# Performance work log

Measured on AMD Instinct MI355X. Metric: run time of the kernel, lower is better.

## Reference

```python
import jax, jax.numpy as jnp
import numpy as np

N = 50000   # nodes
E = 800000  # edges (avg degree 16)
DIMS = [(128, 128), (128, 128), (128, 64)]  # (in, out) per SAGEConv layer
EPS_BN = 1e-5
EPS_NORM = 1e-12


def _make_layer(key, din, dout):
    k1, k2 = jax.random.split(key)
    s = 1.0 / np.sqrt(din)
    return (
        jax.random.normal(k1, (dout, din), jnp.float32) * s,  # Wl: neighbor linear
        jnp.zeros((dout,), jnp.float32),                      # bl
        jax.random.normal(k2, (dout, din), jnp.float32) * s,  # Wr: root linear (no bias in PyG)
        jnp.ones((dout,), jnp.float32),                       # bn gamma
        jnp.zeros((dout,), jnp.float32),                      # bn beta
        jnp.zeros((dout,), jnp.float32),                      # bn running mean
        jnp.ones((dout,), jnp.float32),                       # bn running var
    )


def setup_inputs() -> dict:
    key = jax.random.key(0)
    kx, ke, k0, k1, k2 = jax.random.split(key, 5)
    inp = {
        "x": jax.random.normal(kx, (N, 128), jnp.float32),
        "edge_index": jax.random.randint(ke, (2, E), 0, N, dtype=jnp.int32),
    }
    for i, (k, (din, dout)) in enumerate(zip([k0, k1, k2], DIMS)):
        Wl, bl, Wr, g, b, rm, rv = _make_layer(k, din, dout)
        inp.update({f"Wl{i}": Wl, f"bl{i}": bl, f"Wr{i}": Wr,
                    f"g{i}": g, f"b{i}": b, f"rm{i}": rm, f"rv{i}": rv})
    return inp


def _sage_conv(x, src, dst, Wl, bl, Wr):
    # mean aggregation of incoming messages: gather src features, scatter-add at dst
    agg = jax.ops.segment_sum(x[src], dst, num_segments=N)          # [N, din]
    deg = jax.ops.segment_sum(jnp.ones((src.shape[0],), x.dtype), dst, num_segments=N)
    mean = agg / jnp.maximum(deg, 1.0)[:, None]
    return mean @ Wl.T + bl + x @ Wr.T


def _bn_eval(x, g, b, rm, rv):
    return g * (x - rm) * jax.lax.rsqrt(rv + EPS_BN) + b


def reference(x, edge_index,
              Wl0, bl0, Wr0, g0, b0, rm0, rv0,
              Wl1, bl1, Wr1, g1, b1, rm1, rv1,
              Wl2, bl2, Wr2, g2, b2, rm2, rv2):
    src, dst = edge_index[0], edge_index[1]
    layers = [
        (Wl0, bl0, Wr0, g0, b0, rm0, rv0),
        (Wl1, bl1, Wr1, g1, b1, rm1, rv1),
        (Wl2, bl2, Wr2, g2, b2, rm2, rv2),
    ]
    h = x
    for i, (Wl, bl, Wr, g, b, rm, rv) in enumerate(layers):
        h = _bn_eval(_sage_conv(h, src, dst, Wl, bl, Wr), g, b, rm, rv)
        if i < len(layers) - 1:
            h = jax.nn.relu(h)  # dropout is identity in eval mode
    # F.normalize(p=2, dim=1)
    return h / jnp.maximum(jnp.linalg.norm(h, axis=1, keepdims=True), EPS_NORM)
```

## Files before the change

kernel.cpp:

```cpp
#include <hip/hip_runtime.h>
#include <hip/hip_bf16.h>

#define CDIV(a,b) (((a)+(b)-1)/(b))
#define NBUCK_MAX 512
#define FUSE_CAP 3072

typedef __attribute__((ext_vector_type(8))) short short8;
typedef __attribute__((ext_vector_type(4))) float f32x4;
typedef __attribute__((ext_vector_type(2))) float f32x2;

static __device__ __forceinline__ unsigned short f2bf(float f){
  union { float f; unsigned u; } v; v.f = f;
  unsigned r = v.u + 0x7fffu + ((v.u >> 16) & 1u);
  return (unsigned short)(r >> 16);
}
static __device__ __forceinline__ unsigned pack2(float lo, float hi){
  return (unsigned)f2bf(lo) | ((unsigned)f2bf(hi) << 16);
}
static __device__ __forceinline__ float bf2f(unsigned short s){
  union { unsigned u; float f; } v; v.u = ((unsigned)s) << 16; return v.f;
}
static __device__ __forceinline__ unsigned pk_fp8x4(float a, float b, float c, float d){
  int v = __builtin_amdgcn_cvt_pk_fp8_f32(a, b, 0, false);
  v = __builtin_amdgcn_cvt_pk_fp8_f32(c, d, v, true);
  return (unsigned)v;
}

#define ACCP16(v) { b0 += __builtin_amdgcn_cvt_pk_f32_fp8((int)v.x, false); \
                    b1 += __builtin_amdgcn_cvt_pk_f32_fp8((int)v.x, true);  \
                    b2 += __builtin_amdgcn_cvt_pk_f32_fp8((int)v.y, false); \
                    b3 += __builtin_amdgcn_cvt_pk_f32_fp8((int)v.y, true);  \
                    b4 += __builtin_amdgcn_cvt_pk_f32_fp8((int)v.z, false); \
                    b5 += __builtin_amdgcn_cvt_pk_f32_fp8((int)v.z, true);  \
                    b6 += __builtin_amdgcn_cvt_pk_f32_fp8((int)v.w, false); \
                    b7 += __builtin_amdgcn_cvt_pk_f32_fp8((int)v.w, true); }


struct WtpArgs {
  const float *W0, *W1, *bl, *g, *b, *rm, *rv;
  unsigned short* Bpk; float *sc; float *sh;
  int kblk, dout, do_bn, nblk, perm;
};

static __device__ __forceinline__ void wtp_one(const WtpArgs& a, int idx){
  int NB16 = a.kblk*32*a.dout;
  if (idx < NB16){
    int j = idx & 7, lane = (idx >> 3) & 63, rest = idx >> 9;
    int NT = a.dout >> 4;
    int nt = rest % NT, kk = rest / NT;
    int nn = nt*16 + (lane & 15);
    int k  = kk*32 + ((lane >> 4) * 8) + j;
    float v;
    if (k < 128){
      int kc = a.perm ? (((k & 7) << 4) | (k >> 3)) : k;
      v = a.W0[nn*128 + kc];
    } else {
      v = a.W1[nn*128 + (k - 128)];
    }
    a.Bpk[idx] = f2bf(v);
  } else if (a.do_bn && idx < NB16 + a.dout){
    int jj = idx - NB16;
    float s = a.g[jj] * rsqrtf(a.rv[jj] + 1e-5f);
    a.sc[jj] = s;
    a.sh[jj] = (a.bl[jj] - a.rm[jj]) * s + a.b[jj];
  }
}


__global__ __launch_bounds__(256) void k_prep(const float* __restrict__ x, int n4, unsigned* __restrict__ xb,
                                              unsigned* __restrict__ xq,
                                              const int* __restrict__ dst, int E,
                                              int* __restrict__ bcnt, int nbuck,
                                              int castBlocks, int histBlocks,
                                              WtpArgs a0, WtpArgs a1, WtpArgs a2, WtpArgs a3){
  __shared__ int s[NBUCK_MAX];
  int b = blockIdx.x, t = threadIdx.x;
  if (b < castBlocks){
    int i = b*256 + t;
    if (i < n4){
      float4 v = ((const float4*)x)[i];
      uint2 o; o.x = pack2(v.x, v.y); o.y = pack2(v.z, v.w);
      ((uint2*)xb)[i] = o;
      xq[i] = pk_fp8x4(v.x, v.y, v.z, v.w);
    }
    return;
  }
  b -= castBlocks;
  if (b < histBlocks){
    for (int i=t;i<nbuck;i+=256) s[i] = 0;
    __syncthreads();
    constexpr int EPT = 16;
    int e0 = b*256*EPT;
    #pragma unroll
    for (int i=0;i<EPT;i++){
      int e = e0 + i*256 + t;
      if (e < E) atomicAdd(&s[dst[e] >> 7], 1);
    }
    __syncthreads();
    for (int i=t;i<nbuck;i+=256){
      int c = s[i];
      if (c > 0) atomicAdd(&bcnt[i], c);
    }
    return;
  }
  b -= histBlocks;
  if (b < a0.nblk){ wtp_one(a0, b*256 + t); return; }
  b -= a0.nblk;
  if (b < a1.nblk){ wtp_one(a1, b*256 + t); return; }
  b -= a1.nblk;
  if (b < a2.nblk){ wtp_one(a2, b*256 + t); return; }
  b -= a2.nblk;
  wtp_one(a3, b*256 + t);
}

__global__ __launch_bounds__(256) void k_bucketA(const int* __restrict__ src, const int* __restrict__ dst,
                                                 int E, const int* __restrict__ bcnt,
                                                 int* __restrict__ bcur, unsigned* __restrict__ ebuf, int nbuck){
  __shared__ int scnt[NBUCK_MAX];
  __shared__ int sbase[NBUCK_MAX];
  __shared__ int sboff[NBUCK_MAX];
  __shared__ int ss[256];
  int t = threadIdx.x;
  {
    int a0 = (2*t   < nbuck) ? bcnt[2*t]   : 0;
    int a1 = (2*t+1 < nbuck) ? bcnt[2*t+1] : 0;
    ss[t] = a0 + a1; __syncthreads();
    for (int d=1; d<256; d<<=1){
      int u = (t>=d) ? ss[t-d] : 0;
      __syncthreads();
      ss[t] += u;
      __syncthreads();
    }
    int excl = ss[t] - (a0 + a1);
    if (2*t   < nbuck) sboff[2*t]   = excl;
    if (2*t+1 < nbuck) sboff[2*t+1] = excl + a0;
  }
  for (int i=t;i<nbuck;i+=256) scnt[i] = 0;
  __syncthreads();
  constexpr int EPT = 16;
  int e0 = blockIdx.x*256*EPT;
  int b[EPT]; unsigned pk[EPT];
  #pragma unroll
  for (int i=0;i<EPT;i++){
    int e = e0 + i*256 + t;
    if (e < E){
      int d = dst[e];
      b[i] = d >> 7;
      pk[i] = ((unsigned)(d & 127) << 16) | (unsigned)src[e];
      atomicAdd(&scnt[b[i]], 1);
    } else b[i] = -1;
  }
  __syncthreads();
  for (int i=t;i<nbuck;i+=256){
    int c = scnt[i];
    sbase[i] = (c > 0) ? atomicAdd(&bcur[i], c) : 0;
    scnt[i] = 0;
  }
  __syncthreads();
  #pragma unroll
  for (int i=0;i<EPT;i++){
    if (b[i] >= 0){
      int p = atomicAdd(&scnt[b[i]], 1);
      ebuf[(size_t)sboff[b[i]] + sbase[b[i]] + p] = pk[i];
    }
  }
}


__global__ __launch_bounds__(256, 3) void k_bfuse(
    const unsigned* __restrict__ ebuf, const int* __restrict__ bcnt, int nbuck, int E, int N,
    int* __restrict__ off, int* __restrict__ csr,
    const uint4* __restrict__ xq4, const unsigned short* __restrict__ Ag,
    const unsigned short* __restrict__ Bpk, const float* __restrict__ sc, const float* __restrict__ sh,
    unsigned short* __restrict__ outh, unsigned* __restrict__ outq){
  __shared__ uint4 Ms4[128*17];
  __shared__ int scsr[FUSE_CAP];
  __shared__ int sEx[NBUCK_MAX];
  __shared__ int ss[256];
  unsigned short* Ms = (unsigned short*)Ms4;
  int* sdeg = (int*)Ms4;
  int* sabs = sdeg + 128;
  int* cur  = sabs + 129;
  int b = blockIdx.x, t = threadIdx.x;
  {
    int a0 = (2*t   < nbuck) ? bcnt[2*t]   : 0;
    int a1 = (2*t+1 < nbuck) ? bcnt[2*t+1] : 0;
    ss[t] = a0 + a1; __syncthreads();
    for (int d=1; d<256; d<<=1){
      int u = (t>=d) ? ss[t-d] : 0;
      __syncthreads();
      ss[t] += u;
      __syncthreads();
    }
    int excl = ss[t] - (a0 + a1);
    if (2*t   < nbuck) sEx[2*t]   = excl;
    if (2*t+1 < nbuck) sEx[2*t+1] = excl + a0;
  }
  if (t < 128){ sdeg[t] = 0; cur[t] = 0; }
  __syncthreads();
  int e0 = sEx[b];
  int e1 = (b+1 < nbuck) ? sEx[b+1] : E;
  int span = e1 - e0;
  bool fits = span <= FUSE_CAP;
  for (int e = e0 + t; e < e1; e += 256)
    atomicAdd(&sdeg[ebuf[e] >> 16], 1);
  __syncthreads();
  for (int d=1; d<128; d<<=1){
    int u = (t < 128 && t >= d) ? sdeg[t-d] : 0;
    __syncthreads();
    if (t < 128) sdeg[t] += u;
    __syncthreads();
  }
  if (t == 0) sabs[0] = 0;
  if (t < 128) sabs[t+1] = sdeg[t];
  __syncthreads();
  int n0 = b << 7, n1 = min(n0 + 128, N);
  int cnt = n1 - n0;
  if (t <= cnt) off[n0 + t] = e0 + sabs[t];
  int lane = t & 63, w = t >> 6, sl = lane & 7;
  int gs0[4], gs1[4];
  #pragma unroll
  for (int it=0; it<4; it++){
    int rk = w*32 + it*8 + (lane >> 3);
    gs0[it] = sabs[rk];
    gs1[it] = sabs[rk+1];
  }
  for (int e = e0 + t; e < e1; e += 256){
    unsigned pr = ebuf[e];
    int ln = (int)(pr >> 16);
    int p = atomicAdd(&cur[ln], 1);
    int loc = sabs[ln] + p;
    int sv = (int)(pr & 0xffffu);
    if (fits) scsr[loc] = sv;
    else      csr[e0 + loc] = sv;
  }
  __syncthreads();
  if (fits){
    for (int i = t; i < span; i += 256) csr[e0 + i] = scsr[i];
  } else {
    for (int i = t; i < FUSE_CAP; i += 256) scsr[i] = csr[e0 + i];
    __syncthreads();
  }

  #pragma unroll
  for (int it=0; it<4; it++){
    int rk = w*32 + it*8 + (lane >> 3);
    int s0 = gs0[it], s1 = gs1[it];
    f32x2 b0={0,0},b1={0,0},b2={0,0},b3={0,0},b4={0,0},b5={0,0},b6={0,0},b7={0,0};
    int e = s0;
    for (; e + 8 <= s1; e += 8){
      int i0,i1,i2,i3,i4,i5,i6,i7;
      if (e + 8 <= FUSE_CAP){
        i0 = scsr[e];   i1 = scsr[e+1]; i2 = scsr[e+2]; i3 = scsr[e+3];
        i4 = scsr[e+4]; i5 = scsr[e+5]; i6 = scsr[e+6]; i7 = scsr[e+7];
      } else {
        i0 = csr[e0+e];   i1 = csr[e0+e+1]; i2 = csr[e0+e+2]; i3 = csr[e0+e+3];
        i4 = csr[e0+e+4]; i5 = csr[e0+e+5]; i6 = csr[e0+e+6]; i7 = csr[e0+e+7];
      }
      uint4 v0 = xq4[(size_t)i0*8 + sl];
      uint4 v1 = xq4[(size_t)i1*8 + sl];
      uint4 v2 = xq4[(size_t)i2*8 + sl];
      uint4 v3 = xq4[(size_t)i3*8 + sl];
      uint4 v4 = xq4[(size_t)i4*8 + sl];
      uint4 v5 = xq4[(size_t)i5*8 + sl];
      uint4 v6 = xq4[(size_t)i6*8 + sl];
      uint4 v7 = xq4[(size_t)i7*8 + sl];
      ACCP16(v0); ACCP16(v1); ACCP16(v2); ACCP16(v3);
      ACCP16(v4); ACCP16(v5); ACCP16(v6); ACCP16(v7);
    }
    for (; e + 4 <= s1; e += 4){
      int i0,i1,i2,i3;
      if (e + 4 <= FUSE_CAP){
        i0 = scsr[e]; i1 = scsr[e+1]; i2 = scsr[e+2]; i3 = scsr[e+3];
      } else {
        i0 = csr[e0+e]; i1 = csr[e0+e+1]; i2 = csr[e0+e+2]; i3 = csr[e0+e+3];
      }
      uint4 v0 = xq4[(size_t)i0*8 + sl];
      uint4 v1 = xq4[(size_t)i1*8 + sl];
      uint4 v2 = xq4[(size_t)i2*8 + sl];
      uint4 v3 = xq4[(size_t)i3*8 + sl];
      ACCP16(v0); ACCP16(v1); ACCP16(v2); ACCP16(v3);
    }
    for (; e < s1; e++){
      int ii = (e < FUSE_CAP) ? scsr[e] : csr[e0+e];
      uint4 v = xq4[(size_t)ii*8 + sl];
      ACCP16(v);
    }
    int d = s1 - s0;
    float inv = 1.0f / (float)(d > 0 ? d : 1);
    uint4 o0, o1;
    o0.x = pack2(b0.x*inv, b0.y*inv);  o0.y = pack2(b1.x*inv, b1.y*inv);
    o0.z = pack2(b2.x*inv, b2.y*inv);  o0.w = pack2(b3.x*inv, b3.y*inv);
    o1.x = pack2(b4.x*inv, b4.y*inv);  o1.y = pack2(b5.x*inv, b5.y*inv);
    o1.z = pack2(b6.x*inv, b6.y*inv);  o1.w = pack2(b7.x*inv, b7.y*inv);
    Ms4[rk*17 + sl*2]     = o0;
    Ms4[rk*17 + sl*2 + 1] = o1;
  }
  __syncthreads();

  int quad = lane >> 4, c = lane & 15;
  int mb = n0, woff = w*32;
  int r0 = mb + woff + c;
  int r1 = r0 + 16;

  f32x4 acc[2][8];
  #pragma unroll
  for (int mt=0;mt<2;mt++)
    #pragma unroll
    for (int nt=0;nt<8;nt++) acc[mt][nt] = (f32x4){0.f,0.f,0.f,0.f};

  #pragma unroll
  for (int kk=0; kk<8; kk++){
    int ka = (kk & 3)*32 + quad*8;
    short8 a0, a1;
    if (kk < 4){
      a0 = *(const short8*)&Ms[(woff + c)*136 + ka];
      a1 = *(const short8*)&Ms[(woff + c + 16)*136 + ka];
    } else {
      a0 = (short8){0,0,0,0,0,0,0,0}; a1 = (short8){0,0,0,0,0,0,0,0};
      if (r0 < N) a0 = *(const short8*)(Ag + (size_t)r0*128 + ka);
      if (r1 < N) a1 = *(const short8*)(Ag + (size_t)r1*128 + ka);
    }
    #pragma unroll
    for (int nt=0; nt<8; nt++){
      short8 bb = *(const short8*)(Bpk + (size_t)((kk*8 + nt)*64 + lane)*8);
      acc[0][nt] = __builtin_amdgcn_mfma_f32_16x16x32_bf16(a0, bb, acc[0][nt], 0, 0, 0);
      acc[1][nt] = __builtin_amdgcn_mfma_f32_16x16x32_bf16(a1, bb, acc[1][nt], 0, 0, 0);
    }
  }

  float scv[8], shv[8];
  #pragma unroll
  for (int nt=0;nt<8;nt++){ scv[nt] = sc[nt*16 + c]; shv[nt] = sh[nt*16 + c]; }

  #pragma unroll
  for (int mt=0; mt<2; mt++){
    #pragma unroll
    for (int r=0;r<4;r++){
      int row = mb + woff + mt*16 + quad*4 + r;
      if (row < N){
        float u[8];
        #pragma unroll
        for (int nt=0;nt<8;nt++){
          float uu = acc[mt][nt][r]*scv[nt] + shv[nt];
          u[nt] = fmaxf(uu, 0.f);
          outh[(size_t)row*128 + nt*16 + c] = f2bf(u[nt]);
        }
        uint2 q;
        q.x = pk_fp8x4(u[0], u[1], u[2], u[3]);
        q.y = pk_fp8x4(u[4], u[5], u[6], u[7]);
        ((uint2*)outq)[(size_t)row*16 + c] = q;
      }
    }
  }
}


__global__ __launch_bounds__(256, 3) void k_fuse1(
    const uint4* __restrict__ hq4, const int* __restrict__ off, const int* __restrict__ csr,
    const unsigned short* __restrict__ Ag, const unsigned short* __restrict__ Bpk,
    const float* __restrict__ sc, const float* __restrict__ sh,
    const unsigned short* __restrict__ BpkL,
    unsigned short* __restrict__ outh, unsigned* __restrict__ outyl, int n){
  __shared__ uint4 Ms4[128*17];
  __shared__ uint4 sBL4[1024];
  __shared__ int sw[2];
  unsigned short* Ms = (unsigned short*)Ms4;
  int* scsr = (int*)sBL4;
  int t = threadIdx.x;
  int mb = blockIdx.x*128;
  if (t < 2) sw[t] = off[min(mb + t*128, n)];
  __syncthreads();
  int e0b = sw[0];
  int span = sw[1] - e0b;
  int CAPL = 4096;
  for (int i = t; i < span && i < CAPL; i += 256) scsr[i] = csr[e0b + i];
  __syncthreads();

  int lane = t & 63, w = t >> 6;
  int sl = lane & 7;

  #pragma unroll
  for (int it=0; it<4; it++){
    int rk = w*32 + it*8 + (lane >> 3);
    int idx = mb + rk;
    bool valid = idx < n;
    int s0 = valid ? off[idx]   : 0;
    int s1 = valid ? off[idx+1] : 0;
    f32x2 b0={0,0},b1={0,0},b2={0,0},b3={0,0},b4={0,0},b5={0,0},b6={0,0},b7={0,0};
    int e = s0;
    for (; e + 8 <= s1; e += 8){
      int le = e - e0b;
      int i0,i1,i2,i3,i4,i5,i6,i7;
      if (le + 8 <= CAPL){
        i0 = scsr[le];   i1 = scsr[le+1]; i2 = scsr[le+2]; i3 = scsr[le+3];
        i4 = scsr[le+4]; i5 = scsr[le+5]; i6 = scsr[le+6]; i7 = scsr[le+7];
      } else {
        i0 = csr[e];   i1 = csr[e+1]; i2 = csr[e+2]; i3 = csr[e+3];
        i4 = csr[e+4]; i5 = csr[e+5]; i6 = csr[e+6]; i7 = csr[e+7];
      }
      uint4 v0 = hq4[(size_t)i0*8 + sl];
      uint4 v1 = hq4[(size_t)i1*8 + sl];
      uint4 v2 = hq4[(size_t)i2*8 + sl];
      uint4 v3 = hq4[(size_t)i3*8 + sl];
      uint4 v4 = hq4[(size_t)i4*8 + sl];
      uint4 v5 = hq4[(size_t)i5*8 + sl];
      uint4 v6 = hq4[(size_t)i6*8 + sl];
      uint4 v7 = hq4[(size_t)i7*8 + sl];
      ACCP16(v0); ACCP16(v1); ACCP16(v2); ACCP16(v3);
      ACCP16(v4); ACCP16(v5); ACCP16(v6); ACCP16(v7);
    }
    for (; e + 4 <= s1; e += 4){
      int le = e - e0b;
      int i0,i1,i2,i3;
      if (le + 4 <= CAPL){
        i0 = scsr[le]; i1 = scsr[le+1]; i2 = scsr[le+2]; i3 = scsr[le+3];
      } else {
        i0 = csr[e]; i1 = csr[e+1]; i2 = csr[e+2]; i3 = csr[e+3];
      }
      uint4 v0 = hq4[(size_t)i0*8 + sl];
      uint4 v1 = hq4[(size_t)i1*8 + sl];
      uint4 v2 = hq4[(size_t)i2*8 + sl];
      uint4 v3 = hq4[(size_t)i3*8 + sl];
      ACCP16(v0); ACCP16(v1); ACCP16(v2); ACCP16(v3);
    }
    for (; e < s1; e++){
      int le = e - e0b;
      int ii = (le < CAPL) ? scsr[le] : csr[e];
      uint4 v = hq4[(size_t)ii*8 + sl];
      ACCP16(v);
    }
    int d = s1 - s0;
    float inv = 1.0f / (float)(d > 0 ? d : 1);
    uint4 o0, o1;
    o0.x = pack2(b0.x*inv, b0.y*inv);  o0.y = pack2(b1.x*inv, b1.y*inv);
    o0.z = pack2(b2.x*inv, b2.y*inv);  o0.w = pack2(b3.x*inv, b3.y*inv);
    o1.x = pack2(b4.x*inv, b4.y*inv);  o1.y = pack2(b5.x*inv, b5.y*inv);
    o1.z = pack2(b6.x*inv, b6.y*inv);  o1.w = pack2(b7.x*inv, b7.y*inv);
    Ms4[rk*17 + sl*2]     = o0;
    Ms4[rk*17 + sl*2 + 1] = o1;
  }
  __syncthreads();

  int quad = lane >> 4, c = lane & 15;
  int woff = w*32;
  int r0 = mb + woff + c;
  int r1 = r0 + 16;

  f32x4 acc[2][8];
  #pragma unroll
  for (int mt=0;mt<2;mt++)
    #pragma unroll
    for (int nt=0;nt<8;nt++) acc[mt][nt] = (f32x4){0.f,0.f,0.f,0.f};

  #pragma unroll
  for (int kk=0; kk<8; kk++){
    int ka = (kk & 3)*32 + quad*8;
    short8 a0, a1;
    if (kk < 4){
      a0 = *(const short8*)&Ms[(woff + c)*136 + ka];
      a1 = *(const short8*)&Ms[(woff + c + 16)*136 + ka];
    } else {
      a0 = (short8){0,0,0,0,0,0,0,0}; a1 = (short8){0,0,0,0,0,0,0,0};
      if (r0 < n) a0 = *(const short8*)(Ag + (size_t)r0*128 + ka);
      if (r1 < n) a1 = *(const short8*)(Ag + (size_t)r1*128 + ka);
    }
    #pragma unroll
    for (int nt=0; nt<8; nt++){
      short8 bb = *(const short8*)(Bpk + (size_t)((kk*8 + nt)*64 + lane)*8);
      acc[0][nt] = __builtin_amdgcn_mfma_f32_16x16x32_bf16(a0, bb, acc[0][nt], 0, 0, 0);
      acc[1][nt] = __builtin_amdgcn_mfma_f32_16x16x32_bf16(a1, bb, acc[1][nt], 0, 0, 0);
    }
  }

  float scv[8], shv[8];
  #pragma unroll
  for (int nt=0;nt<8;nt++){ scv[nt] = sc[nt*16 + c]; shv[nt] = sh[nt*16 + c]; }

  __syncthreads();

  #pragma unroll
  for (int mt=0; mt<2; mt++){
    #pragma unroll
    for (int r=0;r<4;r++){
      int lrow = woff + mt*16 + quad*4 + r;
      int row = mb + lrow;
      if (row < n){
        float u[8];
        #pragma unroll
        for (int nt=0;nt<8;nt++){
          float uu = acc[mt][nt][r]*scv[nt] + shv[nt];
          u[nt] = fmaxf(uu, 0.f);
          outh[(size_t)row*128 + nt*16 + c] = f2bf(u[nt]);
        }
        #pragma unroll
        for (int nt=0;nt<8;nt++) Ms[lrow*136 + nt*16 + c] = f2bf(u[nt]);
      } else {
        #pragma unroll
        for (int nt=0;nt<8;nt++) Ms[lrow*136 + nt*16 + c] = 0;
      }
    }
  }

  {
    const uint4* sL = (const uint4*)BpkL;
    #pragma unroll
    for (int i=0;i<4;i++) sBL4[i*256 + t] = sL[i*256 + t];
  }
  __syncthreads();
  unsigned short* BsL = (unsigned short*)sBL4;
  f32x4 acc2[2][4];
  #pragma unroll
  for (int mt=0;mt<2;mt++)
    #pragma unroll
    for (int nt=0;nt<4;nt++) acc2[mt][nt] = (f32x4){0.f,0.f,0.f,0.f};
  int r0l = woff + c, r1l = r0l + 16;
  #pragma unroll
  for (int kk=0; kk<4; kk++){
    int ka = kk*32 + quad*8;
    short8 a0 = *(const short8*)&Ms[r0l*136 + ka];
    short8 a1 = *(const short8*)&Ms[r1l*136 + ka];
    #pragma unroll
    for (int nt=0; nt<4; nt++){
      short8 bb = *(const short8*)&BsL[(size_t)((kk*4 + nt)*64 + lane)*8];
      acc2[0][nt] = __builtin_amdgcn_mfma_f32_16x16x32_bf16(a0, bb, acc2[0][nt], 0, 0, 0);
      acc2[1][nt] = __builtin_amdgcn_mfma_f32_16x16x32_bf16(a1, bb, acc2[1][nt], 0, 0, 0);
    }
  }
  #pragma unroll
  for (int mt=0; mt<2; mt++){
    #pragma unroll
    for (int r=0;r<4;r++){
      int row = mb + woff + mt*16 + quad*4 + r;
      if (row < n){
        unsigned q  = pk_fp8x4(acc2[0][0][r], acc2[0][1][r], acc2[0][2][r], acc2[0][3][r]);
        unsigned q1 = pk_fp8x4(acc2[1][0][r], acc2[1][1][r], acc2[1][2][r], acc2[1][3][r]);
        outyl[(size_t)row*16 + c] = (mt == 0) ? q : q1;
      }
    }
  }
}


#define AGGF_CAP 3072

__global__ __launch_bounds__(256, 3) void k_aggf(
    const uint4* __restrict__ ylq4, const int* __restrict__ off, const int* __restrict__ csr,
    const unsigned short* __restrict__ A0, const unsigned short* __restrict__ BpkR,
    const float* __restrict__ sc, const float* __restrict__ sh,
    float* __restrict__ outf, int n){
  __shared__ unsigned short Ms[128*64];
  __shared__ unsigned short Bs[128*64];
  __shared__ int scsr[AGGF_CAP];
  __shared__ int sw[2];
  int t = threadIdx.x;
  int mb = blockIdx.x*128;
  if (t < 2) sw[t] = off[min(mb + t*128, n)];
  {
    const uint4* s = (const uint4*)BpkR;
    uint4* d = (uint4*)Bs;
    #pragma unroll
    for (int i=0;i<4;i++) d[i*256 + t] = s[i*256 + t];
  }
  __syncthreads();
  int e0b = sw[0];
  int span = sw[1] - e0b;
  for (int i = t; i < span && i < AGGF_CAP; i += 256) scsr[i] = csr[e0b + i];
  __syncthreads();

  int lane = t & 63, w = t >> 6;
  int sl4 = lane & 3;

  #pragma unroll
  for (int it=0; it<2; it++){
    int rk = w*32 + it*16 + (lane >> 2);
    int idx = mb + rk;
    bool valid = idx < n;
    int s0 = valid ? off[idx]   : 0;
    int s1 = valid ? off[idx+1] : 0;
    f32x2 b0={0,0},b1={0,0},b2={0,0},b3={0,0},b4={0,0},b5={0,0},b6={0,0},b7={0,0};
    int e = s0;
    for (; e + 8 <= s1; e += 8){
      int le = e - e0b;
      int i0,i1,i2,i3,i4,i5,i6,i7;
      if (le + 8 <= AGGF_CAP){
        i0 = scsr[le];   i1 = scsr[le+1]; i2 = scsr[le+2]; i3 = scsr[le+3];
        i4 = scsr[le+4]; i5 = scsr[le+5]; i6 = scsr[le+6]; i7 = scsr[le+7];
      } else {
        i0 = csr[e];   i1 = csr[e+1]; i2 = csr[e+2]; i3 = csr[e+3];
        i4 = csr[e+4]; i5 = csr[e+5]; i6 = csr[e+6]; i7 = csr[e+7];
      }
      uint4 v0 = ylq4[(size_t)i0*4 + sl4];
      uint4 v1 = ylq4[(size_t)i1*4 + sl4];
      uint4 v2 = ylq4[(size_t)i2*4 + sl4];
      uint4 v3 = ylq4[(size_t)i3*4 + sl4];
      uint4 v4 = ylq4[(size_t)i4*4 + sl4];
      uint4 v5 = ylq4[(size_t)i5*4 + sl4];
      uint4 v6 = ylq4[(size_t)i6*4 + sl4];
      uint4 v7 = ylq4[(size_t)i7*4 + sl4];
      ACCP16(v0); ACCP16(v1); ACCP16(v2); ACCP16(v3);
      ACCP16(v4); ACCP16(v5); ACCP16(v6); ACCP16(v7);
    }
    for (; e + 4 <= s1; e += 4){
      int le = e - e0b;
      int i0,i1,i2,i3;
      if (le + 4 <= AGGF_CAP){
        i0 = scsr[le]; i1 = scsr[le+1]; i2 = scsr[le+2]; i3 = scsr[le+3];
      } else {
        i0 = csr[e]; i1 = csr[e+1]; i2 = csr[e+2]; i3 = csr[e+3];
      }
      uint4 v0 = ylq4[(size_t)i0*4 + sl4];
      uint4 v1 = ylq4[(size_t)i1*4 + sl4];
      uint4 v2 = ylq4[(size_t)i2*4 + sl4];
      uint4 v3 = ylq4[(size_t)i3*4 + sl4];
      ACCP16(v0); ACCP16(v1); ACCP16(v2); ACCP16(v3);
    }
    for (; e < s1; e++){
      int le = e - e0b;
      int ii = (le < AGGF_CAP) ? scsr[le] : csr[e];
      uint4 v = ylq4[(size_t)ii*4 + sl4];
      ACCP16(v);
    }
    int d = s1 - s0;
    float inv = 1.0f / (float)(d > 0 ? d : 1);
    uint4 o0, o1;
    o0.x = pack2(b0.x*inv, b0.y*inv);  o0.y = pack2(b1.x*inv, b1.y*inv);
    o0.z = pack2(b2.x*inv, b2.y*inv);  o0.w = pack2(b3.x*inv, b3.y*inv);
    o1.x = pack2(b4.x*inv, b4.y*inv);  o1.y = pack2(b5.x*inv, b5.y*inv);
    o1.z = pack2(b6.x*inv, b6.y*inv);  o1.w = pack2(b7.x*inv, b7.y*inv);
    ((uint4*)Ms)[rk*8 + sl4*2]     = o0;
    ((uint4*)Ms)[rk*8 + sl4*2 + 1] = o1;
  }
  __syncthreads();

  int quad = lane >> 4, c = lane & 15;
  int woff = w*32;
  int r0 = mb + woff + c;
  int r1 = r0 + 16;
  f32x4 acc[2][4];
  #pragma unroll
  for (int mt=0;mt<2;mt++)
    #pragma unroll
    for (int nt=0;nt<4;nt++) acc[mt][nt] = (f32x4){0.f,0.f,0.f,0.f};
  #pragma unroll
  for (int kk=0; kk<4; kk++){
    int ka = kk*32 + quad*8;
    short8 a0 = {0,0,0,0,0,0,0,0}, a1 = {0,0,0,0,0,0,0,0};
    if (r0 < n) a0 = *(const short8*)(A0 + (size_t)r0*128 + ka);
    if (r1 < n) a1 = *(const short8*)(A0 + (size_t)r1*128 + ka);
    #pragma unroll
    for (int nt=0; nt<4; nt++){
      short8 bb = *(const short8*)&Bs[(size_t)((kk*4 + nt)*64 + lane)*8];
      acc[0][nt] = __builtin_amdgcn_mfma_f32_16x16x32_bf16(a0, bb, acc[0][nt], 0, 0, 0);
      acc[1][nt] = __builtin_amdgcn_mfma_f32_16x16x32_bf16(a1, bb, acc[1][nt], 0, 0, 0);
    }
  }

  float scv[4], shv[4];
  #pragma unroll
  for (int nt=0;nt<4;nt++){ scv[nt] = sc[nt*16 + c]; shv[nt] = sh[nt*16 + c]; }

  #pragma unroll
  for (int mt=0; mt<2; mt++){
    #pragma unroll
    for (int r=0;r<4;r++){
      int lr = woff + mt*16 + quad*4 + r;
      int row = mb + lr;
      float v[4];
      float ss = 0.f;
      if (row < n){
        #pragma unroll
        for (int nt=0;nt<4;nt++){
          float u = acc[mt][nt][r] + bf2f(Ms[lr*64 + c*4 + nt]);
          u = u*scv[nt] + shv[nt];
          v[nt] = u;
          ss += u*u;
        }
      } else {
        #pragma unroll
        for (int nt=0;nt<4;nt++) v[nt] = 0.f;
      }
      ss += __shfl_xor(ss, 1, 64);
      ss += __shfl_xor(ss, 2, 64);
      ss += __shfl_xor(ss, 4, 64);
      ss += __shfl_xor(ss, 8, 64);
      float rn = 1.0f / fmaxf(sqrtf(ss), 1e-12f);
      if (row < n){
        #pragma unroll
        for (int nt=0;nt<4;nt++) outf[(size_t)row*64 + nt*16 + c] = v[nt]*rn;
      }
    }
  }
}


extern "C" void kernel_launch(void* const* d_in, const int* in_sizes, int n_in,
                              void* d_out, int out_size, void* d_ws, size_t ws_size,
                              hipStream_t stream){
  const float* x = (const float*)d_in[0];
  const int* ei  = (const int*)d_in[1];
  int N = in_sizes[0] / 128;
  int E = in_sizes[1] / 2;
  const int* esrc = ei;
  const int* edst = ei + E;
  int nbuck = CDIV(N, 128);

  const float *Wl[3], *bl[3], *Wr[3], *g[3], *bb[3], *rm[3], *rv[3];
  int dout[3];
  for (int i=0;i<3;i++){
    int base = 2 + 7*i;
    Wl[i]=(const float*)d_in[base];   bl[i]=(const float*)d_in[base+1];
    Wr[i]=(const float*)d_in[base+2]; g[i] =(const float*)d_in[base+3];
    bb[i]=(const float*)d_in[base+4]; rm[i]=(const float*)d_in[base+5];
    rv[i]=(const float*)d_in[base+6];
    dout[i] = in_sizes[base] / 128;
  }

  char* p = (char*)d_ws;
  size_t o = 0;
  auto alloc = [&](size_t bytes)->void*{ void* r = p + o; o += (bytes + 255) & ~(size_t)255; return r; };
  int* bz    = (int*)alloc((size_t)2*nbuck*4);
  int* bcnt  = bz;
  int* bcur  = bz + nbuck;
  int* off   = (int*)alloc((size_t)(N+1)*4);
  int* csr   = (int*)alloc((size_t)E*4);
  unsigned* ebuf = (unsigned*)alloc((size_t)E*4);
  unsigned* xb   = (unsigned*)alloc((size_t)N*64*4);
  unsigned* xq   = (unsigned*)alloc((size_t)N*128);
  unsigned* h_a  = (unsigned*)alloc((size_t)N*64*4);
  unsigned* haq  = (unsigned*)alloc((size_t)N*128);
  unsigned* h_b  = (unsigned*)alloc((size_t)N*64*4);
  unsigned* ylb  = (unsigned*)alloc((size_t)N*64);
  unsigned short* Bpk01[2];
  float* sc[3]; float* sh[3];
  for (int i=0;i<2;i++) Bpk01[i] = (unsigned short*)alloc((size_t)256*dout[i]*2);
  unsigned short* BpkL = (unsigned short*)alloc((size_t)128*dout[2]*2);
  unsigned short* BpkR = (unsigned short*)alloc((size_t)128*dout[2]*2);
  for (int i=0;i<3;i++){
    sc[i] = (float*)alloc((size_t)dout[i]*4);
    sh[i] = (float*)alloc((size_t)dout[i]*4);
  }

  hipMemsetAsync(bz, 0, (size_t)2*nbuck*4, stream);

  WtpArgs wa[4];
  wa[0] = { Wl[0], Wr[0], bl[0], g[0], bb[0], rm[0], rv[0], Bpk01[0], sc[0], sh[0], 8, dout[0], 1, CDIV(256*dout[0]+dout[0],256), 0 };
  wa[1] = { Wl[1], Wr[1], bl[1], g[1], bb[1], rm[1], rv[1], Bpk01[1], sc[1], sh[1], 8, dout[1], 1, CDIV(256*dout[1]+dout[1],256), 1 };
  wa[2] = { Wl[2], nullptr, nullptr, nullptr, nullptr, nullptr, nullptr, BpkL, nullptr, nullptr, 4, dout[2], 0, CDIV(128*dout[2],256), 0 };
  wa[3] = { Wr[2], nullptr, bl[2], g[2], bb[2], rm[2], rv[2], BpkR, sc[2], sh[2], 4, dout[2], 1, CDIV(128*dout[2]+dout[2],256), 0 };

  int castBlocks = CDIV(N*32, 256);
  int histBlocks = CDIV(E, 256*16);
  int prepBlocks = castBlocks + histBlocks + wa[0].nblk + wa[1].nblk + wa[2].nblk + wa[3].nblk;
  k_prep   <<<prepBlocks,256,0,stream>>>(x, N*32, xb, xq, edst, E, bcnt, nbuck, castBlocks, histBlocks,
                                         wa[0], wa[1], wa[2], wa[3]);
  k_bucketA<<<CDIV(E,256*16),256,0,stream>>>(esrc, edst, E, bcnt, bcur, ebuf, nbuck);

  k_bfuse<<<nbuck,256,0,stream>>>(ebuf, bcnt, nbuck, E, N, off, csr,
                                  (const uint4*)xq, (const unsigned short*)xb,
                                  Bpk01[0], sc[0], sh[0],
                                  (unsigned short*)h_a, haq);
  k_fuse1<<<nbuck,256,0,stream>>>((const uint4*)haq, off, csr,
                                  (const unsigned short*)h_a, Bpk01[1], sc[1], sh[1], BpkL,
                                  (unsigned short*)h_b, ylb, N);
  k_aggf<<<nbuck,256,0,stream>>>((const uint4*)ylb, off, csr,
                                 (const unsigned short*)h_b, BpkR, sc[2], sh[2],
                                 (float*)d_out, N);
}
```

Before: 236.1 us.

## Split each 128-node bucket into two 64-node blocks across fused kernels

Each of the three layer kernels now launches two blocks per 128-node bucket, and each block handles 64 nodes with one 16-row MFMA tile per wave instead of two. The bucket-fuse kernel still scans the whole bucket's edges but only places those whose local node falls in its half, writing CSR at half-relative offsets. The goal is more blocks (about 782 instead of 391) and smaller LDS footprints, for better occupancy and load balance across CUs. The cost is that both halves redundantly scan the bucket edges, prefix-sums and degree counts, and each block reuses its weight loads less.

```diff
diff --git a/kernel.cpp b/kernel.cpp
--- a/kernel.cpp
+++ b/kernel.cpp
@@ -3,7 +3,9 @@
 
 #define CDIV(a,b) (((a)+(b)-1)/(b))
 #define NBUCK_MAX 512
-#define FUSE_CAP 3072
+#define FUSE_CAP 1536
+#define CAPL     4096
+#define AGGF_CAP 2048
 
 typedef __attribute__((ext_vector_type(8))) short short8;
 typedef __attribute__((ext_vector_type(4))) float f32x4;
@@ -173,7 +175,7 @@
     const uint4* __restrict__ xq4, const unsigned short* __restrict__ Ag,
     const unsigned short* __restrict__ Bpk, const float* __restrict__ sc, const float* __restrict__ sh,
     unsigned short* __restrict__ outh, unsigned* __restrict__ outq){
-  __shared__ uint4 Ms4[128*17];
+  __shared__ uint4 Ms4[64*17];
   __shared__ int scsr[FUSE_CAP];
   __shared__ int sEx[NBUCK_MAX];
   __shared__ int ss[256];
@@ -181,7 +183,9 @@
   int* sdeg = (int*)Ms4;
   int* sabs = sdeg + 128;
   int* cur  = sabs + 129;
-  int b = blockIdx.x, t = threadIdx.x;
+  int bb_ = blockIdx.x;
+  int b = bb_ >> 1, hi = bb_ & 1;
+  int t = threadIdx.x;
   {
     int a0 = (2*t   < nbuck) ? bcnt[2*t]   : 0;
     int a1 = (2*t+1 < nbuck) ? bcnt[2*t+1] : 0;
@@ -200,8 +204,6 @@
   __syncthreads();
   int e0 = sEx[b];
   int e1 = (b+1 < nbuck) ? sEx[b+1] : E;
-  int span = e1 - e0;
-  bool fits = span <= FUSE_CAP;
   for (int e = e0 + t; e < e1; e += 256)
     atomicAdd(&sdeg[ebuf[e] >> 16], 1);
   __syncthreads();
@@ -214,37 +216,43 @@
   if (t == 0) sabs[0] = 0;
   if (t < 128) sabs[t+1] = sdeg[t];
   __syncthreads();
-  int n0 = b << 7, n1 = min(n0 + 128, N);
-  int cnt = n1 - n0;
-  if (t <= cnt) off[n0 + t] = e0 + sabs[t];
+  int base64 = sabs[hi*64];
+  int myTot  = sabs[hi*64 + 64] - base64;
+  int n0 = (b << 7) + hi*64;
+  int cnt = (N > n0) ? min(64, N - n0) : 0;
+  if (cnt > 0 && t <= cnt) off[n0 + t] = e0 + sabs[hi*64 + t];
   int lane = t & 63, w = t >> 6, sl = lane & 7;
-  int gs0[4], gs1[4];
-  #pragma unroll
-  for (int it=0; it<4; it++){
-    int rk = w*32 + it*8 + (lane >> 3);
-    gs0[it] = sabs[rk];
-    gs1[it] = sabs[rk+1];
-  }
+  int gs0[2], gs1[2];
+  #pragma unroll
+  for (int it=0; it<2; it++){
+    int rk = w*16 + it*8 + (lane >> 3);
+    gs0[it] = sabs[hi*64 + rk] - base64;
+    gs1[it] = sabs[hi*64 + rk + 1] - base64;
+  }
+  bool fits = myTot <= FUSE_CAP;
   for (int e = e0 + t; e < e1; e += 256){
     unsigned pr = ebuf[e];
     int ln = (int)(pr >> 16);
-    int p = atomicAdd(&cur[ln], 1);
-    int loc = sabs[ln] + p;
-    int sv = (int)(pr & 0xffffu);
-    if (fits) scsr[loc] = sv;
-    else      csr[e0 + loc] = sv;
-  }
-  __syncthreads();
+    if ((ln >> 6) == hi){
+      int p = atomicAdd(&cur[ln], 1);
+      int gpos = sabs[ln] + p;
+      int sv = (int)(pr & 0xffffu);
+      if (fits) scsr[gpos - base64] = sv;
+      else      csr[e0 + gpos] = sv;
+    }
+  }
+  __syncthreads();
+  const int* gcsr = csr + e0 + base64;
   if (fits){
-    for (int i = t; i < span; i += 256) csr[e0 + i] = scsr[i];
+    for (int i = t; i < myTot; i += 256) csr[e0 + base64 + i] = scsr[i];
   } else {
-    for (int i = t; i < FUSE_CAP; i += 256) scsr[i] = csr[e0 + i];
+    for (int i = t; i < FUSE_CAP; i += 256) scsr[i] = gcsr[i];
     __syncthreads();
   }
 
   #pragma unroll
-  for (int it=0; it<4; it++){
-    int rk = w*32 + it*8 + (lane >> 3);
+  for (int it=0; it<2; it++){
+    int rk = w*16 + it*8 + (lane >> 3);
     int s0 = gs0[it], s1 = gs1[it];
     f32x2 b0={0,0},b1={0,0},b2={0,0},b3={0,0},b4={0,0},b5={0,0},b6={0,0},b7={0,0};
     int e = s0;
@@ -254,8 +262,8 @@
         i0 = scsr[e];   i1 = scsr[e+1]; i2 = scsr[e+2]; i3 = scsr[e+3];
         i4 = scsr[e+4]; i5 = scsr[e+5]; i6 = scsr[e+6]; i7 = scsr[e+7];
       } else {
-        i0 = csr[e0+e];   i1 = csr[e0+e+1]; i2 = csr[e0+e+2]; i3 = csr[e0+e+3];
-        i4 = csr[e0+e+4]; i5 = csr[e0+e+5]; i6 = csr[e0+e+6]; i7 = csr[e0+e+7];
+        i0 = gcsr[e];   i1 = gcsr[e+1]; i2 = gcsr[e+2]; i3 = gcsr[e+3];
+        i4 = gcsr[e+4]; i5 = gcsr[e+5]; i6 = gcsr[e+6]; i7 = gcsr[e+7];
       }
       uint4 v0 = xq4[(size_t)i0*8 + sl];
       uint4 v1 = xq4[(size_t)i1*8 + sl];
@@ -273,7 +281,7 @@
       if (e + 4 <= FUSE_CAP){
         i0 = scsr[e]; i1 = scsr[e+1]; i2 = scsr[e+2]; i3 = scsr[e+3];
       } else {
-        i0 = csr[e0+e]; i1 = csr[e0+e+1]; i2 = csr[e0+e+2]; i3 = csr[e0+e+3];
+        i0 = gcsr[e]; i1 = gcsr[e+1]; i2 = gcsr[e+2]; i3 = gcsr[e+3];
       }
       uint4 v0 = xq4[(size_t)i0*8 + sl];
       uint4 v1 = xq4[(size_t)i1*8 + sl];
@@ -282,7 +290,7 @@
       ACCP16(v0); ACCP16(v1); ACCP16(v2); ACCP16(v3);
     }
     for (; e < s1; e++){
-      int ii = (e < FUSE_CAP) ? scsr[e] : csr[e0+e];
+      int ii = (e < FUSE_CAP) ? scsr[e] : gcsr[e];
       uint4 v = xq4[(size_t)ii*8 + sl];
       ACCP16(v);
     }
@@ -299,33 +307,27 @@
   __syncthreads();
 
   int quad = lane >> 4, c = lane & 15;
-  int mb = n0, woff = w*32;
-  int r0 = mb + woff + c;
-  int r1 = r0 + 16;
-
-  f32x4 acc[2][8];
-  #pragma unroll
-  for (int mt=0;mt<2;mt++)
-    #pragma unroll
-    for (int nt=0;nt<8;nt++) acc[mt][nt] = (f32x4){0.f,0.f,0.f,0.f};
+  int woff = w*16;
+  int r0 = n0 + woff + c;
+
+  f32x4 acc[8];
+  #pragma unroll
+  for (int nt=0;nt<8;nt++) acc[nt] = (f32x4){0.f,0.f,0.f,0.f};
 
   #pragma unroll
   for (int kk=0; kk<8; kk++){
     int ka = (kk & 3)*32 + quad*8;
-    short8 a0, a1;
+    short8 a0;
     if (kk < 4){
       a0 = *(const short8*)&Ms[(woff + c)*136 + ka];
-      a1 = *(const short8*)&Ms[(woff + c + 16)*136 + ka];
     } else {
-      a0 = (short8){0,0,0,0,0,0,0,0}; a1 = (short8){0,0,0,0,0,0,0,0};
+      a0 = (short8){0,0,0,0,0,0,0,0};
       if (r0 < N) a0 = *(const short8*)(Ag + (size_t)r0*128 + ka);
-      if (r1 < N) a1 = *(const short8*)(Ag + (size_t)r1*128 + ka);
     }
     #pragma unroll
     for (int nt=0; nt<8; nt++){
-      short8 bb = *(const short8*)(Bpk + (size_t)((kk*8 + nt)*64 + lane)*8);
-      acc[0][nt] = __builtin_amdgcn_mfma_f32_16x16x32_bf16(a0, bb, acc[0][nt], 0, 0, 0);
-      acc[1][nt] = __builtin_amdgcn_mfma_f32_16x16x32_bf16(a1, bb, acc[1][nt], 0, 0, 0);
+      short8 bb2 = *(const short8*)(Bpk + (size_t)((kk*8 + nt)*64 + lane)*8);
+      acc[nt] = __builtin_amdgcn_mfma_f32_16x16x32_bf16(a0, bb2, acc[nt], 0, 0, 0);
     }
   }
 
@@ -334,23 +336,20 @@
   for (int nt=0;nt<8;nt++){ scv[nt] = sc[nt*16 + c]; shv[nt] = sh[nt*16 + c]; }
 
   #pragma unroll
-  for (int mt=0; mt<2; mt++){
-    #pragma unroll
-    for (int r=0;r<4;r++){
-      int row = mb + woff + mt*16 + quad*4 + r;
-      if (row < N){
-        float u[8];
-        #pragma unroll
-        for (int nt=0;nt<8;nt++){
-          float uu = acc[mt][nt][r]*scv[nt] + shv[nt];
-          u[nt] = fmaxf(uu, 0.f);
-          outh[(size_t)row*128 + nt*16 + c] = f2bf(u[nt]);
-        }
-        uint2 q;
-        q.x = pk_fp8x4(u[0], u[1], u[2], u[3]);
-        q.y = pk_fp8x4(u[4], u[5], u[6], u[7]);
-        ((uint2*)outq)[(size_t)row*16 + c] = q;
-      }
+  for (int r=0;r<4;r++){
+    int row = n0 + woff + quad*4 + r;
+    if (row < N){
+      float u[8];
+      #pragma unroll
+      for (int nt=0;nt<8;nt++){
+        float uu = acc[nt][r]*scv[nt] + shv[nt];
+        u[nt] = fmaxf(uu, 0.f);
+        outh[(size_t)row*128 + nt*16 + c] = f2bf(u[nt]);
+      }
+      uint2 q;
+      q.x = pk_fp8x4(u[0], u[1], u[2], u[3]);
+      q.y = pk_fp8x4(u[4], u[5], u[6], u[7]);
+      ((uint2*)outq)[(size_t)row*16 + c] = q;
     }
   }
 }
@@ -362,18 +361,17 @@
     const float* __restrict__ sc, const float* __restrict__ sh,
     const unsigned short* __restrict__ BpkL,
     unsigned short* __restrict__ outh, unsigned* __restrict__ outyl, int n){
-  __shared__ uint4 Ms4[128*17];
+  __shared__ uint4 Ms4[64*17];
   __shared__ uint4 sBL4[1024];
   __shared__ int sw[2];
   unsigned short* Ms = (unsigned short*)Ms4;
   int* scsr = (int*)sBL4;
   int t = threadIdx.x;
-  int mb = blockIdx.x*128;
-  if (t < 2) sw[t] = off[min(mb + t*128, n)];
+  int n0 = blockIdx.x*64;
+  if (t < 2) sw[t] = off[min(n0 + t*64, n)];
   __syncthreads();
   int e0b = sw[0];
   int span = sw[1] - e0b;
-  int CAPL = 4096;
   for (int i = t; i < span && i < CAPL; i += 256) scsr[i] = csr[e0b + i];
   __syncthreads();
 
@@ -381,9 +379,9 @@
   int sl = lane & 7;
 
   #pragma unroll
-  for (int it=0; it<4; it++){
-    int rk = w*32 + it*8 + (lane >> 3);
-    int idx = mb + rk;
+  for (int it=0; it<2; it++){
+    int rk = w*16 + it*8 + (lane >> 3);
+    int idx = n0 + rk;
     bool valid = idx < n;
     int s0 = valid ? off[idx]   : 0;
     int s1 = valid ? off[idx+1] : 0;
@@ -443,33 +441,27 @@
   __syncthreads();
 
   int quad = lane >> 4, c = lane & 15;
-  int woff = w*32;
-  int r0 = mb + woff + c;
-  int r1 = r0 + 16;
-
-  f32x4 acc[2][8];
-  #pragma unroll
-  for (int mt=0;mt<2;mt++)
-    #pragma unroll
-    for (int nt=0;nt<8;nt++) acc[mt][nt] = (f32x4){0.f,0.f,0.f,0.f};
+  int woff = w*16;
+  int r0 = n0 + woff + c;
+
+  f32x4 acc[8];
+  #pragma unroll
+  for (int nt=0;nt<8;nt++) acc[nt] = (f32x4){0.f,0.f,0.f,0.f};
 
   #pragma unroll
   for (int kk=0; kk<8; kk++){
     int ka = (kk & 3)*32 + quad*8;
-    short8 a0, a1;
+    short8 a0;
     if (kk < 4){
       a0 = *(const short8*)&Ms[(woff + c)*136 + ka];
-      a1 = *(const short8*)&Ms[(woff + c + 16)*136 + ka];
     } else {
-      a0 = (short8){0,0,0,0,0,0,0,0}; a1 = (short8){0,0,0,0,0,0,0,0};
+      a0 = (short8){0,0,0,0,0,0,0,0};
       if (r0 < n) a0 = *(const short8*)(Ag + (size_t)r0*128 + ka);
-      if (r1 < n) a1 = *(const short8*)(Ag + (size_t)r1*128 + ka);
     }
     #pragma unroll
     for (int nt=0; nt<8; nt++){
-      short8 bb = *(const short8*)(Bpk + (size_t)((kk*8 + nt)*64 + lane)*8);
-      acc[0][nt] = __builtin_amdgcn_mfma_f32_16x16x32_bf16(a0, bb, acc[0][nt], 0, 0, 0);
-      acc[1][nt] = __builtin_amdgcn_mfma_f32_16x16x32_bf16(a1, bb, acc[1][nt], 0, 0, 0);
+      short8 bb2 = *(const short8*)(Bpk + (size_t)((kk*8 + nt)*64 + lane)*8);
+      acc[nt] = __builtin_amdgcn_mfma_f32_16x16x32_bf16(a0, bb2, acc[nt], 0, 0, 0);
     }
   }
 
@@ -480,25 +472,22 @@
   __syncthreads();
 
   #pragma unroll
-  for (int mt=0; mt<2; mt++){
-    #pragma unroll
-    for (int r=0;r<4;r++){
-      int lrow = woff + mt*16 + quad*4 + r;
-      int row = mb + lrow;
-      if (row < n){
-        float u[8];
-        #pragma unroll
-        for (int nt=0;nt<8;nt++){
-          float uu = acc[mt][nt][r]*scv[nt] + shv[nt];
-          u[nt] = fmaxf(uu, 0.f);
-          outh[(size_t)row*128 + nt*16 + c] = f2bf(u[nt]);
-        }
-        #pragma unroll
-        for (int nt=0;nt<8;nt++) Ms[lrow*136 + nt*16 + c] = f2bf(u[nt]);
-      } else {
-        #pragma unroll
-        for (int nt=0;nt<8;nt++) Ms[lrow*136 + nt*16 + c] = 0;
-      }
+  for (int r=0;r<4;r++){
+    int lrow = woff + quad*4 + r;
+    int row = n0 + lrow;
+    if (row < n){
+      float u[8];
+      #pragma unroll
+      for (int nt=0;nt<8;nt++){
+        float uu = acc[nt][r]*scv[nt] + shv[nt];
+        u[nt] = fmaxf(uu, 0.f);
+        outh[(size_t)row*128 + nt*16 + c] = f2bf(u[nt]);
+      }
+      #pragma unroll
+      for (int nt=0;nt<8;nt++) Ms[lrow*136 + nt*16 + c] = f2bf(u[nt]);
+    } else {
+      #pragma unroll
+      for (int nt=0;nt<8;nt++) Ms[lrow*136 + nt*16 + c] = 0;
     }
   }
 
@@ -509,53 +498,43 @@
   }
   __syncthreads();
   unsigned short* BsL = (unsigned short*)sBL4;
-  f32x4 acc2[2][4];
-  #pragma unroll
-  for (int mt=0;mt<2;mt++)
-    #pragma unroll
-    for (int nt=0;nt<4;nt++) acc2[mt][nt] = (f32x4){0.f,0.f,0.f,0.f};
-  int r0l = woff + c, r1l = r0l + 16;
+  f32x4 acc2[4];
+  #pragma unroll
+  for (int nt=0;nt<4;nt++) acc2[nt] = (f32x4){0.f,0.f,0.f,0.f};
+  int r0l = woff + c;
   #pragma unroll
   for (int kk=0; kk<4; kk++){
     int ka = kk*32 + quad*8;
     short8 a0 = *(const short8*)&Ms[r0l*136 + ka];
-    short8 a1 = *(const short8*)&Ms[r1l*136 + ka];
     #pragma unroll
     for (int nt=0; nt<4; nt++){
-      short8 bb = *(const short8*)&BsL[(size_t)((kk*4 + nt)*64 + lane)*8];
-      acc2[0][nt] = __builtin_amdgcn_mfma_f32_16x16x32_bf16(a0, bb, acc2[0][nt], 0, 0, 0);
-      acc2[1][nt] = __builtin_amdgcn_mfma_f32_16x16x32_bf16(a1, bb, acc2[1][nt], 0, 0, 0);
-    }
-  }
-  #pragma unroll
-  for (int mt=0; mt<2; mt++){
-    #pragma unroll
-    for (int r=0;r<4;r++){
-      int row = mb + woff + mt*16 + quad*4 + r;
-      if (row < n){
-        unsigned q  = pk_fp8x4(acc2[0][0][r], acc2[0][1][r], acc2[0][2][r], acc2[0][3][r]);
-        unsigned q1 = pk_fp8x4(acc2[1][0][r], acc2[1][1][r], acc2[1][2][r], acc2[1][3][r]);
-        outyl[(size_t)row*16 + c] = (mt == 0) ? q : q1;
-      }
-    }
-  }
-}
-
-
-#define AGGF_CAP 3072
+      short8 bb2 = *(const short8*)&BsL[(size_t)((kk*4 + nt)*64 + lane)*8];
+      acc2[nt] = __builtin_amdgcn_mfma_f32_16x16x32_bf16(a0, bb2, acc2[nt], 0, 0, 0);
+    }
+  }
+  #pragma unroll
+  for (int r=0;r<4;r++){
+    int row = n0 + woff + quad*4 + r;
+    if (row < n){
+      unsigned q = pk_fp8x4(acc2[0][r], acc2[1][r], acc2[2][r], acc2[3][r]);
+      outyl[(size_t)row*16 + c] = q;
+    }
+  }
+}
+
 
 __global__ __launch_bounds__(256, 3) void k_aggf(
     const uint4* __restrict__ ylq4, const int* __restrict__ off, const int* __restrict__ csr,
     const unsigned short* __restrict__ A0, const unsigned short* __restrict__ BpkR,
     const float* __restrict__ sc, const float* __restrict__ sh,
     float* __restrict__ outf, int n){
-  __shared__ unsigned short Ms[128*64];
+  __shared__ unsigned short Ms[64*64];
   __shared__ unsigned short Bs[128*64];
   __shared__ int scsr[AGGF_CAP];
   __shared__ int sw[2];
   int t = threadIdx.x;
-  int mb = blockIdx.x*128;
-  if (t < 2) sw[t] = off[min(mb + t*128, n)];
+  int n0 = blockIdx.x*64;
+  if (t < 2) sw[t] = off[min(n0 + t*64, n)];
   {
     const uint4* s = (const uint4*)BpkR;
     uint4* d = (uint4*)Bs;
@@ -571,10 +550,9 @@
   int lane = t & 63, w = t >> 6;
   int sl4 = lane & 3;
 
-  #pragma unroll
-  for (int it=0; it<2; it++){
-    int rk = w*32 + it*16 + (lane >> 2);
-    int idx = mb + rk;
+  {
+    int rk = w*16 + (lane >> 2);
+    int idx = n0 + rk;
     bool valid = idx < n;
     int s0 = valid ? off[idx]   : 0;
     int s1 = valid ? off[idx+1] : 0;
@@ -634,25 +612,20 @@
   __syncthreads();
 
   int quad = lane >> 4, c = lane & 15;
-  int woff = w*32;
-  int r0 = mb + woff + c;
-  int r1 = r0 + 16;
-  f32x4 acc[2][4];
-  #pragma unroll
-  for (int mt=0;mt<2;mt++)
-    #pragma unroll
-    for (int nt=0;nt<4;nt++) acc[mt][nt] = (f32x4){0.f,0.f,0.f,0.f};
+  int woff = w*16;
+  int r0 = n0 + woff + c;
+  f32x4 acc[4];
+  #pragma unroll
+  for (int nt=0;nt<4;nt++) acc[nt] = (f32x4){0.f,0.f,0.f,0.f};
   #pragma unroll
   for (int kk=0; kk<4; kk++){
     int ka = kk*32 + quad*8;
-    short8 a0 = {0,0,0,0,0,0,0,0}, a1 = {0,0,0,0,0,0,0,0};
+    short8 a0 = {0,0,0,0,0,0,0,0};
     if (r0 < n) a0 = *(const short8*)(A0 + (size_t)r0*128 + ka);
-    if (r1 < n) a1 = *(const short8*)(A0 + (size_t)r1*128 + ka);
     #pragma unroll
     for (int nt=0; nt<4; nt++){
-      short8 bb = *(const short8*)&Bs[(size_t)((kk*4 + nt)*64 + lane)*8];
-      acc[0][nt] = __builtin_amdgcn_mfma_f32_16x16x32_bf16(a0, bb, acc[0][nt], 0, 0, 0);
-      acc[1][nt] = __builtin_amdgcn_mfma_f32_16x16x32_bf16(a1, bb, acc[1][nt], 0, 0, 0);
+      short8 bb2 = *(const short8*)&Bs[(size_t)((kk*4 + nt)*64 + lane)*8];
+      acc[nt] = __builtin_amdgcn_mfma_f32_16x16x32_bf16(a0, bb2, acc[nt], 0, 0, 0);
     }
   }
 
@@ -661,34 +634,31 @@
   for (int nt=0;nt<4;nt++){ scv[nt] = sc[nt*16 + c]; shv[nt] = sh[nt*16 + c]; }
 
   #pragma unroll
-  for (int mt=0; mt<2; mt++){
-    #pragma unroll
-    for (int r=0;r<4;r++){
-      int lr = woff + mt*16 + quad*4 + r;
-      int row = mb + lr;
-      float v[4];
-      float ss = 0.f;
-      if (row < n){
-        #pragma unroll
-        for (int nt=0;nt<4;nt++){
-          float u = acc[mt][nt][r] + bf2f(Ms[lr*64 + c*4 + nt]);
-          u = u*scv[nt] + shv[nt];
-          v[nt] = u;
-          ss += u*u;
-        }
-      } else {
-        #pragma unroll
-        for (int nt=0;nt<4;nt++) v[nt] = 0.f;
-      }
-      ss += __shfl_xor(ss, 1, 64);
-      ss += __shfl_xor(ss, 2, 64);
-      ss += __shfl_xor(ss, 4, 64);
-      ss += __shfl_xor(ss, 8, 64);
-      float rn = 1.0f / fmaxf(sqrtf(ss), 1e-12f);
-      if (row < n){
-        #pragma unroll
-        for (int nt=0;nt<4;nt++) outf[(size_t)row*64 + nt*16 + c] = v[nt]*rn;
-      }
+  for (int r=0;r<4;r++){
+    int lr = woff + quad*4 + r;
+    int row = n0 + lr;
+    float v[4];
+    float ss2 = 0.f;
+    if (row < n){
+      #pragma unroll
+      for (int nt=0;nt<4;nt++){
+        float u = acc[nt][r] + bf2f(Ms[lr*64 + c*4 + nt]);
+        u = u*scv[nt] + shv[nt];
+        v[nt] = u;
+        ss2 += u*u;
+      }
+    } else {
+      #pragma unroll
+      for (int nt=0;nt<4;nt++) v[nt] = 0.f;
+    }
+    ss2 += __shfl_xor(ss2, 1, 64);
+    ss2 += __shfl_xor(ss2, 2, 64);
+    ss2 += __shfl_xor(ss2, 4, 64);
+    ss2 += __shfl_xor(ss2, 8, 64);
+    float rn = 1.0f / fmaxf(sqrtf(ss2), 1e-12f);
+    if (row < n){
+      #pragma unroll
+      for (int nt=0;nt<4;nt++) outf[(size_t)row*64 + nt*16 + c] = v[nt]*rn;
     }
   }
 }
@@ -704,6 +674,7 @@
   const int* esrc = ei;
   const int* edst = ei + E;
   int nbuck = CDIV(N, 128);
+  int nb2 = 2*nbuck;
 
   const float *Wl[3], *bl[3], *Wr[3], *g[3], *bb[3], *rm[3], *rv[3];
   int dout[3];
@@ -756,14 +727,14 @@
                                          wa[0], wa[1], wa[2], wa[3]);
   k_bucketA<<<CDIV(E,256*16),256,0,stream>>>(esrc, edst, E, bcnt, bcur, ebuf, nbuck);
 
-  k_bfuse<<<nbuck,256,0,stream>>>(ebuf, bcnt, nbuck, E, N, off, csr,
-                                  (const uint4*)xq, (const unsigned short*)xb,
-                                  Bpk01[0], sc[0], sh[0],
-                                  (unsigned short*)h_a, haq);
-  k_fuse1<<<nbuck,256,0,stream>>>((const uint4*)haq, off, csr,
-                                  (const unsigned short*)h_a, Bpk01[1], sc[1], sh[1], BpkL,
-                                  (unsigned short*)h_b, ylb, N);
-  k_aggf<<<nbuck,256,0,stream>>>((const uint4*)ylb, off, csr,
-                                 (const unsigned short*)h_b, BpkR, sc[2], sh[2],
-                                 (float*)d_out, N);
-}
+  k_bfuse<<<nb2,256,0,stream>>>(ebuf, bcnt, nbuck, E, N, off, csr,
+                                (const uint4*)xq, (const unsigned short*)xb,
+                                Bpk01[0], sc[0], sh[0],
+                                (unsigned short*)h_a, haq);
+  k_fuse1<<<nb2,256,0,stream>>>((const uint4*)haq, off, csr,
+                                (const unsigned short*)h_a, Bpk01[1], sc[1], sh[1], BpkL,
+                                (unsigned short*)h_b, ylb, N);
+  k_aggf<<<nb2,256,0,stream>>>((const uint4*)ylb, off, csr,
+                               (const unsigned short*)h_b, BpkR, sc[2], sh[2],
+                               (float*)d_out, N);
+}
```

New measurement: 226.0 us. 1.04x faster.
